# Kernel tuning notes

Hardware: AMD Instinct MI355X
Metric: run time of the kernel (lower is better)

The kernel has to match this reference:

```python
import jax, jax.numpy as jnp
import numpy as np

N_NODES = 100000
N_EDGES = 3200000
N_GRAPHS = 512
HID = 64
OUT = 10


def setup_inputs() -> dict:
    key = jax.random.key(0)
    ks = jax.random.split(key, 10)
    x = jax.random.normal(ks[0], (N_NODES,), dtype=jnp.float32)
    edge_index = jax.random.randint(ks[1], (2, N_EDGES), 0, N_NODES, dtype=jnp.int64)
    batch = jnp.sort(jax.random.randint(ks[2], (N_NODES,), 0, N_GRAPHS, dtype=jnp.int64))
    # GCNConv weights (glorot) and zero biases, Linear layer params
    W1 = jax.random.normal(ks[3], (1, HID), dtype=jnp.float32) * (1.0 / np.sqrt(1 + HID))
    b1 = jnp.zeros((HID,), dtype=jnp.float32)
    W2 = jax.random.normal(ks[4], (HID, HID), dtype=jnp.float32) * (1.0 / np.sqrt(2 * HID))
    b2 = jnp.zeros((HID,), dtype=jnp.float32)
    Wl = jax.random.normal(ks[5], (2 * HID, OUT), dtype=jnp.float32) * (1.0 / np.sqrt(2 * HID))
    bl = jnp.zeros((OUT,), dtype=jnp.float32)
    return {"x": x, "edge_index": edge_index, "batch": batch,
            "W1": W1, "b1": b1, "W2": W2, "b2": b2, "Wl": Wl, "bl": bl}


def reference(x, edge_index, batch, W1, b1, W2, b2, Wl, bl):
    N = x.shape[0]
    loop = jnp.arange(N, dtype=edge_index.dtype)
    src = jnp.concatenate([edge_index[0], loop])  # add self-loops
    dst = jnp.concatenate([edge_index[1], loop])
    # symmetric GCN normalization: D^{-1/2} A_hat D^{-1/2}
    deg = jax.ops.segment_sum(jnp.ones_like(dst, dtype=jnp.float32), dst, num_segments=N)
    dinv = jax.lax.rsqrt(jnp.maximum(deg, 1.0))
    norm = (dinv[src] * dinv[dst])[:, None]  # [E+N, 1]

    def gcn(h, W, b):
        m = (h @ W)[src] * norm  # transform then gather messages
        return jax.ops.segment_sum(m, dst, num_segments=N) + b

    h0 = x[:, None]  # [N, 1] (dropout is identity at eval)
    x1 = jax.nn.relu(gcn(h0, W1, b1))
    x2 = jax.nn.relu(gcn(x1, W2, b2))
    xj = jnp.concatenate([x1, x2], axis=-1)  # JK 'cat' -> [N, 128]
    # global mean pool per graph
    cnt = jax.ops.segment_sum(jnp.ones((N,), jnp.float32), batch, num_segments=N_GRAPHS)
    pooled = jax.ops.segment_sum(xj, batch, num_segments=N_GRAPHS) / jnp.maximum(cnt, 1.0)[:, None]
    return pooled @ Wl + bl  # [G, 10]
```

## Files before the change

### kernel.cpp

```cpp
#include <hip/hip_runtime.h>
#include <hip/hip_bf16.h>

#define N_NODES 100000
#define N_EDGES 3200000
#define N_GRAPHS 512
#define HID 64
#define OUT_DIM 10

#define NPB 98
#define NB  1021
#define CAP 3584

__global__ __launch_bounds__(256) void k_part(const int4* __restrict__ src4,
                                              const int4* __restrict__ dst4,
                                              unsigned* __restrict__ bcur,
                                              unsigned* __restrict__ ebuf) {
    __shared__ unsigned hist[NB];
    __shared__ unsigned curs[NB];
    int tid = threadIdx.x;
    for (int i = tid; i < NB; i += 256) hist[i] = 0;
    __syncthreads();
    int4 s[4], d[4];
    int base4 = (blockIdx.x * 256 + tid) * 4;
    #pragma unroll
    for (int k = 0; k < 4; k++) {
        int i4 = base4 + k;
        if (i4 < N_EDGES / 4) { s[k] = src4[i4]; d[k] = dst4[i4]; }
        else { s[k] = make_int4(-1, -1, -1, -1); d[k] = make_int4(0, 0, 0, 0); }
    }
    #pragma unroll
    for (int k = 0; k < 4; k++) {
        if (s[k].x >= 0) {
            atomicAdd(&hist[d[k].x / NPB], 1u);
            atomicAdd(&hist[d[k].y / NPB], 1u);
            atomicAdd(&hist[d[k].z / NPB], 1u);
            atomicAdd(&hist[d[k].w / NPB], 1u);
        }
    }
    __syncthreads();
    for (int b = tid; b < NB; b += 256) {
        unsigned c = hist[b];
        curs[b] = c ? atomicAdd(&bcur[b], c) : 0u;
    }
    __syncthreads();
    #pragma unroll
    for (int k = 0; k < 4; k++) {
        if (s[k].x >= 0) {
            int ss[4] = { s[k].x, s[k].y, s[k].z, s[k].w };
            int dd[4] = { d[k].x, d[k].y, d[k].z, d[k].w };
            #pragma unroll
            for (int m = 0; m < 4; m++) {
                int b = dd[m] / NPB;
                unsigned dl = (unsigned)(dd[m] - b * NPB);
                unsigned slot = atomicAdd(&curs[b], 1u);
                ebuf[(size_t)b * CAP + slot] = (dl << 24) | (unsigned)ss[m];
            }
        }
    }
}

__global__ __launch_bounds__(256) void k_buck1(const unsigned* __restrict__ ebuf,
                                               const unsigned* __restrict__ bcur,
                                               const float* __restrict__ x,
                                               unsigned* __restrict__ deg,
                                               float* __restrict__ dinv,
                                               float* __restrict__ g1) {
    __shared__ unsigned cnt[NPB];
    int b = blockIdx.x, tid = threadIdx.x;
    if (tid < NPB) cnt[tid] = 0;
    __syncthreads();
    int ec = (int)bcur[b];
    const unsigned* eb = ebuf + (size_t)b * CAP;
    for (int i = tid; i < ec; i += 256)
        atomicAdd(&cnt[eb[i] >> 24], 1u);
    __syncthreads();
    int n0 = b * NPB;
    int nn = min(NPB, N_NODES - n0);
    if (tid < nn) {
        unsigned c = cnt[tid];
        float dn = 1.0f / sqrtf((float)c + 1.0f);
        deg[n0 + tid] = c;
        dinv[n0 + tid] = dn;
        g1[n0 + tid] = dn * x[n0 + tid];
    }
}

__global__ __launch_bounds__(256) void k_buck2(const unsigned* __restrict__ ebuf,
                                               const unsigned* __restrict__ bcur,
                                               const float* __restrict__ g1,
                                               const float* __restrict__ dinv,
                                               const float* __restrict__ x,
                                               float2* __restrict__ sd) {
    __shared__ float sacc[NPB];
    int b = blockIdx.x, tid = threadIdx.x;
    if (tid < NPB) sacc[tid] = 0.f;
    __syncthreads();
    int ec = (int)bcur[b];
    const unsigned* eb = ebuf + (size_t)b * CAP;
    for (int i = tid; i < ec; i += 256) {
        unsigned w = eb[i];
        atomicAdd(&sacc[w >> 24], g1[w & 0x00FFFFFFu]);
    }
    __syncthreads();
    int n0 = b * NPB;
    int nn = min(NPB, N_NODES - n0);
    if (tid < nn) {
        float dn = dinv[n0 + tid];
        float s = dn * (sacc[tid] + dn * x[n0 + tid]);
        sd[n0 + tid] = make_float2(s, dn);
    }
}

__global__ __launch_bounds__(256) void k_buck3(const unsigned* __restrict__ ebuf,
                                               const unsigned* __restrict__ bcur,
                                               const unsigned* __restrict__ deg,
                                               const float2* __restrict__ sd,
                                               const float* __restrict__ W1,
                                               const float* __restrict__ b1,
                                               const float* __restrict__ W2,
                                               const float* __restrict__ b2,
                                               float* __restrict__ x2) {
    __shared__ unsigned sorted[CAP];
    __shared__ float2 stage[256];
    __shared__ int offs[NPB + 1];
    __shared__ unsigned curs[NPB];
    int b = blockIdx.x, tid = threadIdx.x;
    int lane = tid & 63, wv = tid >> 6;
    int n0 = b * NPB;
    int nn = min(NPB, N_NODES - n0);
    if (tid == 0) {
        int r = 0;
        for (int i = 0; i < nn; i++) { offs[i] = r; curs[i] = (unsigned)r; r += (int)deg[n0 + i]; }
        offs[nn] = r;
    }
    float w2col[HID];
    #pragma unroll
    for (int j = 0; j < HID; j++) w2col[j] = W2[j * HID + lane];
    float w1 = W1[lane], bb1 = b1[lane], bb2 = b2[lane];
    __syncthreads();
    int ec = (int)bcur[b];
    const unsigned* eb = ebuf + (size_t)b * CAP;
    for (int i = tid; i < ec; i += 256) {
        unsigned w = eb[i];
        unsigned slot = atomicAdd(&curs[w >> 24], 1u);
        sorted[slot] = w;
    }
    __syncthreads();
    float2* st = stage + wv * 64;
    for (int n = wv; n < nn; n += 4) {
        int lo = offs[n], hi = offs[n + 1];
        float acca = 0.f, accb = 0.f;
        for (int base = lo; base < hi; base += 64) {
            int m = hi - base; if (m > 64) m = 64;
            float2 v = make_float2(0.f, 0.f);
            if (lane < m) v = sd[sorted[base + lane] & 0x00FFFFFFu];
            st[lane] = v;
            int k = 0;
            for (; k + 1 < m; k += 2) {
                float2 e0 = st[k];
                float2 e1 = st[k + 1];
                acca = fmaf(e0.y, fmaxf(fmaf(e0.x, w1, bb1), 0.f), acca);
                accb = fmaf(e1.y, fmaxf(fmaf(e1.x, w1, bb1), 0.f), accb);
            }
            if (k < m) {
                float2 e0 = st[k];
                acca = fmaf(e0.y, fmaxf(fmaf(e0.x, w1, bb1), 0.f), acca);
            }
        }
        float2 self = sd[n0 + n];
        float t = fmaxf(fmaf(self.x, w1, bb1), 0.f);
        float a = self.y * (acca + accb + self.y * t);
        float acc2a = bb2, acc2b = 0.f;
        #pragma unroll
        for (int j = 0; j < HID; j += 2) {
            float aj0 = __int_as_float(__builtin_amdgcn_readlane(__float_as_int(a), j));
            float aj1 = __int_as_float(__builtin_amdgcn_readlane(__float_as_int(a), j + 1));
            acc2a = fmaf(aj0, w2col[j], acc2a);
            acc2b = fmaf(aj1, w2col[j + 1], acc2b);
        }
        x2[(size_t)(n0 + n) * HID + lane] = fmaxf(acc2a + acc2b, 0.f);
    }
}

__global__ void k_bounds(const int* __restrict__ batch, int* __restrict__ gstart) {
    int i = blockIdx.x * blockDim.x + threadIdx.x;
    if (i >= N_NODES) return;
    int b = batch[i];
    if (i == 0) {
        for (int g = 0; g <= b; g++) gstart[g] = 0;
    } else {
        int pb = batch[i - 1];
        for (int g = pb + 1; g <= b; g++) gstart[g] = i;
    }
    if (i == N_NODES - 1) {
        for (int g = b + 1; g <= N_GRAPHS; g++) gstart[g] = N_NODES;
    }
}

__global__ __launch_bounds__(256) void k_pool(const float* __restrict__ x2,
                                              const float2* __restrict__ sd,
                                              const float* __restrict__ W1,
                                              const float* __restrict__ b1,
                                              const int* __restrict__ gstart,
                                              const float* __restrict__ Wl,
                                              const float* __restrict__ bl,
                                              float* __restrict__ out) {
    int g = blockIdx.x;
    int t = threadIdx.x;
    int c = t & 127;
    int part = t >> 7;
    int lo = gstart[g], hi = gstart[g + 1];
    float w = 0.f, b = 0.f;
    if (c < HID) { w = W1[c]; b = b1[c]; }
    float acc = 0.f;
    if (c < HID) {
        for (int n = lo + part; n < hi; n += 2)
            acc += fmaxf(fmaf(sd[n].x, w, b), 0.f);
    } else {
        int j = c - HID;
        for (int n = lo + part; n < hi; n += 2)
            acc += x2[(size_t)n * HID + j];
    }
    __shared__ float pl[2 * HID];
    if (part == 0) pl[c] = acc;
    __syncthreads();
    if (part == 1) pl[c] += acc;
    __syncthreads();
    if (t < 2 * HID) pl[t] /= fmaxf((float)(hi - lo), 1.f);
    __syncthreads();
    if (t < OUT_DIM) {
        float r = bl[t];
        #pragma unroll 16
        for (int j = 0; j < 2 * HID; j++) r = fmaf(pl[j], Wl[j * OUT_DIM + t], r);
        out[g * OUT_DIM + t] = r;
    }
}

extern "C" void kernel_launch(void* const* d_in, const int* in_sizes, int n_in,
                              void* d_out, int out_size, void* d_ws, size_t ws_size,
                              hipStream_t stream) {
    const float* x      = (const float*)d_in[0];
    const int*   ei     = (const int*)d_in[1];
    const int*   batch  = (const int*)d_in[2];
    const float* W1     = (const float*)d_in[3];
    const float* b1     = (const float*)d_in[4];
    const float* W2     = (const float*)d_in[5];
    const float* b2     = (const float*)d_in[6];
    const float* Wl     = (const float*)d_in[7];
    const float* bl     = (const float*)d_in[8];
    float* out = (float*)d_out;

    const int* src = ei;
    const int* dst = ei + N_EDGES;

    char* p = (char*)d_ws;
    auto alloc = [&](size_t bytes) { void* r = (void*)p; p += (bytes + 255) & ~(size_t)255; return r; };
    unsigned* bcur   = (unsigned*)alloc(NB * 4);
    unsigned* ebuf   = (unsigned*)alloc((size_t)NB * CAP * 4);
    unsigned* deg    = (unsigned*)alloc(N_NODES * 4);
    float*    dinv   = (float*)alloc(N_NODES * 4);
    float*    g1     = (float*)alloc(N_NODES * 4);
    float2*   sd     = (float2*)alloc((size_t)N_NODES * 8);
    float*    x2     = (float*)alloc((size_t)N_NODES * HID * 4);
    int*      gstart = (int*)alloc((N_GRAPHS + 1) * 4);

    hipMemsetAsync(bcur, 0, NB * 4, stream);

    const int TB = 256;
    int pbl = (N_EDGES / 16 + TB - 1) / TB;
    int nbl = (N_NODES + TB - 1) / TB;

    k_part <<<pbl, TB, 0, stream>>>((const int4*)src, (const int4*)dst, bcur, ebuf);
    k_buck1<<<NB, TB, 0, stream>>>(ebuf, bcur, x, deg, dinv, g1);
    k_buck2<<<NB, TB, 0, stream>>>(ebuf, bcur, g1, dinv, x, sd);
    k_buck3<<<NB, TB, 0, stream>>>(ebuf, bcur, deg, sd, W1, b1, W2, b2, x2);
    k_bounds<<<nbl, TB, 0, stream>>>(batch, gstart);
    k_pool <<<N_GRAPHS, TB, 0, stream>>>(x2, sd, W1, b1, gstart, Wl, bl, out);
}
```

Baseline: 262.2 us.

## Fuse mean-pool accumulation into layer-2 kernel, drop x2 buffer

The layer-2 kernel now accumulates per-graph sums of the layer-1 and layer-2 activations in registers while walking nodes. Because batch is sorted, it flushes each sum to global pooled buffers with atomics only when the graph id changes. This removes the 25.6 MB x2 write and its re-read in the pool kernel, which becomes a small head kernel. The partition kernel also processes half as many edges per thread with twice the blocks. The trade-offs are extra atomics, two added memsets, and run-to-run nondeterminism in float summation order.

```diff
diff --git a/kernel.cpp b/kernel.cpp
--- a/kernel.cpp
+++ b/kernel.cpp
@@ -20,16 +20,16 @@
     int tid = threadIdx.x;
     for (int i = tid; i < NB; i += 256) hist[i] = 0;
     __syncthreads();
-    int4 s[4], d[4];
-    int base4 = (blockIdx.x * 256 + tid) * 4;
-    #pragma unroll
-    for (int k = 0; k < 4; k++) {
+    int4 s[2], d[2];
+    int base4 = (blockIdx.x * 256 + tid) * 2;
+    #pragma unroll
+    for (int k = 0; k < 2; k++) {
         int i4 = base4 + k;
         if (i4 < N_EDGES / 4) { s[k] = src4[i4]; d[k] = dst4[i4]; }
         else { s[k] = make_int4(-1, -1, -1, -1); d[k] = make_int4(0, 0, 0, 0); }
     }
     #pragma unroll
-    for (int k = 0; k < 4; k++) {
+    for (int k = 0; k < 2; k++) {
         if (s[k].x >= 0) {
             atomicAdd(&hist[d[k].x / NPB], 1u);
             atomicAdd(&hist[d[k].y / NPB], 1u);
@@ -44,7 +44,7 @@
     }
     __syncthreads();
     #pragma unroll
-    for (int k = 0; k < 4; k++) {
+    for (int k = 0; k < 2; k++) {
         if (s[k].x >= 0) {
             int ss[4] = { s[k].x, s[k].y, s[k].z, s[k].w };
             int dd[4] = { d[k].x, d[k].y, d[k].z, d[k].w };
@@ -115,11 +115,13 @@
                                                const unsigned* __restrict__ bcur,
                                                const unsigned* __restrict__ deg,
                                                const float2* __restrict__ sd,
+                                               const int* __restrict__ batch,
                                                const float* __restrict__ W1,
                                                const float* __restrict__ b1,
                                                const float* __restrict__ W2,
                                                const float* __restrict__ b2,
-                                               float* __restrict__ x2) {
+                                               float* __restrict__ pooled1,
+                                               float* __restrict__ pooled2) {
     __shared__ unsigned sorted[CAP];
     __shared__ float2 stage[256];
     __shared__ int offs[NPB + 1];
@@ -147,6 +149,8 @@
     }
     __syncthreads();
     float2* st = stage + wv * 64;
+    int curg = -1;
+    float pacc1 = 0.f, pacc2 = 0.f;
     for (int n = wv; n < nn; n += 4) {
         int lo = offs[n], hi = offs[n + 1];
         float acca = 0.f, accb = 0.f;
@@ -178,7 +182,21 @@
             acc2a = fmaf(aj0, w2col[j], acc2a);
             acc2b = fmaf(aj1, w2col[j + 1], acc2b);
         }
-        x2[(size_t)(n0 + n) * HID + lane] = fmaxf(acc2a + acc2b, 0.f);
+        float x2v = fmaxf(acc2a + acc2b, 0.f);
+        int g = batch[n0 + n];
+        if (g != curg) {
+            if (curg >= 0) {
+                atomicAdd(&pooled1[curg * HID + lane], pacc1);
+                atomicAdd(&pooled2[curg * HID + lane], pacc2);
+            }
+            curg = g; pacc1 = 0.f; pacc2 = 0.f;
+        }
+        pacc1 += t;
+        pacc2 += x2v;
+    }
+    if (curg >= 0) {
+        atomicAdd(&pooled1[curg * HID + lane], pacc1);
+        atomicAdd(&pooled2[curg * HID + lane], pacc2);
     }
 }
 
@@ -197,36 +215,18 @@
     }
 }
 
-__global__ __launch_bounds__(256) void k_pool(const float* __restrict__ x2,
-                                              const float2* __restrict__ sd,
-                                              const float* __restrict__ W1,
-                                              const float* __restrict__ b1,
+__global__ __launch_bounds__(128) void k_head(const float* __restrict__ pooled1,
+                                              const float* __restrict__ pooled2,
                                               const int* __restrict__ gstart,
                                               const float* __restrict__ Wl,
                                               const float* __restrict__ bl,
                                               float* __restrict__ out) {
     int g = blockIdx.x;
     int t = threadIdx.x;
-    int c = t & 127;
-    int part = t >> 7;
-    int lo = gstart[g], hi = gstart[g + 1];
-    float w = 0.f, b = 0.f;
-    if (c < HID) { w = W1[c]; b = b1[c]; }
-    float acc = 0.f;
-    if (c < HID) {
-        for (int n = lo + part; n < hi; n += 2)
-            acc += fmaxf(fmaf(sd[n].x, w, b), 0.f);
-    } else {
-        int j = c - HID;
-        for (int n = lo + part; n < hi; n += 2)
-            acc += x2[(size_t)n * HID + j];
-    }
+    float denom = fmaxf((float)(gstart[g + 1] - gstart[g]), 1.f);
     __shared__ float pl[2 * HID];
-    if (part == 0) pl[c] = acc;
-    __syncthreads();
-    if (part == 1) pl[c] += acc;
-    __syncthreads();
-    if (t < 2 * HID) pl[t] /= fmaxf((float)(hi - lo), 1.f);
+    if (t < HID) pl[t] = pooled1[g * HID + t] / denom;
+    else         pl[t] = pooled2[g * HID + (t - HID)] / denom;
     __syncthreads();
     if (t < OUT_DIM) {
         float r = bl[t];
@@ -255,25 +255,28 @@
 
     char* p = (char*)d_ws;
     auto alloc = [&](size_t bytes) { void* r = (void*)p; p += (bytes + 255) & ~(size_t)255; return r; };
-    unsigned* bcur   = (unsigned*)alloc(NB * 4);
-    unsigned* ebuf   = (unsigned*)alloc((size_t)NB * CAP * 4);
-    unsigned* deg    = (unsigned*)alloc(N_NODES * 4);
-    float*    dinv   = (float*)alloc(N_NODES * 4);
-    float*    g1     = (float*)alloc(N_NODES * 4);
-    float2*   sd     = (float2*)alloc((size_t)N_NODES * 8);
-    float*    x2     = (float*)alloc((size_t)N_NODES * HID * 4);
-    int*      gstart = (int*)alloc((N_GRAPHS + 1) * 4);
+    unsigned* bcur    = (unsigned*)alloc(NB * 4);
+    unsigned* ebuf    = (unsigned*)alloc((size_t)NB * CAP * 4);
+    unsigned* deg     = (unsigned*)alloc(N_NODES * 4);
+    float*    dinv    = (float*)alloc(N_NODES * 4);
+    float*    g1      = (float*)alloc(N_NODES * 4);
+    float2*   sd      = (float2*)alloc((size_t)N_NODES * 8);
+    float*    pooled1 = (float*)alloc((size_t)N_GRAPHS * HID * 4);
+    float*    pooled2 = (float*)alloc((size_t)N_GRAPHS * HID * 4);
+    int*      gstart  = (int*)alloc((N_GRAPHS + 1) * 4);
 
     hipMemsetAsync(bcur, 0, NB * 4, stream);
+    hipMemsetAsync(pooled1, 0, (size_t)N_GRAPHS * HID * 4, stream);
+    hipMemsetAsync(pooled2, 0, (size_t)N_GRAPHS * HID * 4, stream);
 
     const int TB = 256;
-    int pbl = (N_EDGES / 16 + TB - 1) / TB;
+    int pbl = (N_EDGES / 8 + TB - 1) / TB;
     int nbl = (N_NODES + TB - 1) / TB;
 
     k_part <<<pbl, TB, 0, stream>>>((const int4*)src, (const int4*)dst, bcur, ebuf);
     k_buck1<<<NB, TB, 0, stream>>>(ebuf, bcur, x, deg, dinv, g1);
     k_buck2<<<NB, TB, 0, stream>>>(ebuf, bcur, g1, dinv, x, sd);
-    k_buck3<<<NB, TB, 0, stream>>>(ebuf, bcur, deg, sd, W1, b1, W2, b2, x2);
     k_bounds<<<nbl, TB, 0, stream>>>(batch, gstart);
-    k_pool <<<N_GRAPHS, TB, 0, stream>>>(x2, sd, W1, b1, gstart, Wl, bl, out);
-}
+    k_buck3<<<NB, TB, 0, stream>>>(ebuf, bcur, deg, sd, batch, W1, b1, W2, b2, pooled1, pooled2);
+    k_head <<<N_GRAPHS, 128, 0, stream>>>(pooled1, pooled2, gstart, Wl, bl, out);
+}
```

Measured after the change: 257.0 us. 2.0% less time.
